# Optimization experiments

Measured on AMD Instinct MI355X. Metric: run time of the kernel, lower is better.

The kernel has to match this reference:

```python
import jax, jax.numpy as jnp
import numpy as np


def _masked(scores, mask):
    return jnp.where(mask == 0, -jnp.inf, scores)


def setup_inputs() -> dict:
    key = jax.random.key(0)
    ks = jax.random.split(key, 4)
    B, H, S, D = 2, 12, 4096, 64
    blk = 64
    nb = S // blk          # 64 blocks
    nw = nb - 2            # 62 windows
    R = 3                  # random blocks per window
    return {
        'query': jax.random.normal(ks[0], (B, H, S, D), dtype=jnp.float32),
        'key': jax.random.normal(ks[1], (B, H, S, D), dtype=jnp.float32),
        'value': jax.random.normal(ks[2], (B, H, S, D), dtype=jnp.float32),
        'q_mask': jnp.ones((B, 1, S, 1), dtype=jnp.float32),
        'kv_mask': jnp.ones((B, 1, 1, S), dtype=jnp.float32),
        'band_mask': jnp.ones((B, 1, nb - 4, blk, 3 * blk), dtype=jnp.float32),
        'q_block_mask': jnp.ones((B, nb, blk), dtype=jnp.float32),
        'kv_block_mask': jnp.ones((B, nb, blk), dtype=jnp.float32),
        'random_attn': jax.random.randint(ks[3], (H, nw, R), 0, nb, dtype=jnp.int32),
        'q_block_size': blk,
        'kv_block_size': blk,
    }


def reference(query, key, value, q_mask, kv_mask, band_mask, q_block_mask,
              kv_block_mask, random_attn, q_block_size, kv_block_size):
    B, H, S, D = query.shape
    Skv = key.shape[2]
    qb, kb = q_block_size, kv_block_size
    nb, nkb = S // qb, Skv // kb
    scale = 1.0 / (D ** 0.5)

    # expand random indices over batch: [B,H,nw,R]
    ra = jnp.broadcast_to(random_attn[None].astype(jnp.int32),
                          (B,) + random_attn.shape)
    nw, R = ra.shape[2], ra.shape[3]
    bidx = jnp.arange(B)[:, None, None, None]
    hidx = jnp.arange(H)[None, :, None, None]

    # random mask: [B,H,nw,qb,R*kb]
    rm = kv_block_mask[bidx, ra].reshape(B, H, nw, R * kb)
    random_mask = jnp.einsum('blq,bhlk->bhlqk', q_block_mask[:, 1:-1], rm)

    bq = query.reshape(B, H, nb, qb, D)
    bk = key.reshape(B, H, nkb, kb, D)
    bv = value.reshape(B, H, nkb, kb, D)

    # gathered random blocks: [B,H,nw,R*kb,D]
    sk = bk[bidx, hidx, ra].reshape(B, H, nw, R * kb, D)
    sv = bv[bidx, hidx, ra].reshape(B, H, nw, R * kb, D)

    # --- first query block: attends to everything ---
    p1 = jnp.einsum('bhqd,bhkd->bhqk', bq[:, :, 0], key) * scale
    a1 = jax.nn.softmax(_masked(p1, kv_mask), axis=-1)
    c1 = jnp.einsum('bhqk,bhkd->bhqd', a1, value)[:, :, None]

    # --- second query block ---
    k2 = jnp.concatenate([bk[:, :, 0], bk[:, :, 1], bk[:, :, 2], bk[:, :, -1],
                          sk[:, :, 0]], axis=2)
    v2 = jnp.concatenate([bv[:, :, 0], bv[:, :, 1], bv[:, :, 2], bv[:, :, -1],
                          sv[:, :, 0]], axis=2)
    p2 = jnp.einsum('bhqd,bhkd->bhqk', bq[:, :, 1], k2) * scale
    seq_pad = jnp.concatenate([kv_mask[:, :, :, :3 * kb],
                               kv_mask[:, :, :, -kb:],
                               jnp.ones_like(random_mask[:, :1, 0, :1])], axis=3)
    rand_pad = jnp.concatenate([jnp.ones_like(p2[:, :, :, :4 * kb]),
                                random_mask[:, :, 0]], axis=3)
    a2 = jax.nn.softmax(_masked(p2, jnp.minimum(seq_pad, rand_pad)), axis=-1)
    c2 = jnp.einsum('bhqk,bhkd->bhqd', a2, v2)[:, :, None]

    # --- middle blocks: window + global(first,last) + random ---
    ebk = jnp.concatenate([bk[:, :, 1:-3], bk[:, :, 2:-2], bk[:, :, 3:-1]], axis=3)
    ebv = jnp.concatenate([bv[:, :, 1:-3], bv[:, :, 2:-2], bv[:, :, 3:-1]], axis=3)
    mq = bq[:, :, 2:-2]  # [B,H,nb-4,qb,D]
    inner = _masked(jnp.einsum('bhlqd,bhlkd->bhlqk', mq, ebk) * scale, band_mask)
    randp = _masked(jnp.einsum('bhlqd,bhlkd->bhlqk', mq, sk[:, :, 1:-1]) * scale,
                    random_mask[:, :, 1:-1])
    fop = _masked(jnp.einsum('bhlqd,bhkd->bhlqk', mq, bk[:, :, 0]) * scale,
                  kv_mask[:, :, :, :kb][:, :, :, None, :])
    lop = _masked(jnp.einsum('bhlqd,bhkd->bhlqk', mq, bk[:, :, -1]) * scale,
                  kv_mask[:, :, :, -kb:][:, :, :, None, :])
    band = jnp.concatenate([fop, inner, lop, randp], axis=-1)
    aw = jax.nn.softmax(band, axis=-1)
    cm = jnp.einsum('bhlqk,bhlkd->bhlqd', aw[..., kb:4 * kb], ebv)
    cm += jnp.einsum('bhlqk,bhlkd->bhlqd', aw[..., 4 * kb:-kb], sv[:, :, 1:-1])
    cm += jnp.einsum('bhlqk,bhkd->bhlqd', aw[..., :kb], bv[:, :, 0])
    cm += jnp.einsum('bhlqk,bhkd->bhlqd', aw[..., -kb:], bv[:, :, -1])

    # --- second-to-last query block ---
    k3 = jnp.concatenate([bk[:, :, 0], bk[:, :, -3], bk[:, :, -2], bk[:, :, -1],
                          sk[:, :, -1]], axis=2)
    v3 = jnp.concatenate([bv[:, :, 0], bv[:, :, -3], bv[:, :, -2], bv[:, :, -1],
                          sv[:, :, -1]], axis=2)
    p3 = jnp.einsum('bhqd,bhkd->bhqk', bq[:, :, -2], k3) * scale
    seq_pad3 = jnp.concatenate([kv_mask[:, :, :, :kb],
                                kv_mask[:, :, :, -3 * kb:],
                                jnp.ones_like(random_mask[:, :1, 0, :1])], axis=3)
    rand_pad3 = jnp.concatenate([jnp.ones_like(p3[:, :, :, :4 * kb]),
                                 random_mask[:, :, -1]], axis=3)
    a3 = jax.nn.softmax(_masked(p3, jnp.minimum(seq_pad3, rand_pad3)), axis=-1)
    c3 = jnp.einsum('bhqk,bhkd->bhqd', a3, v3)[:, :, None]

    # --- last query block: attends to everything ---
    p4 = jnp.einsum('bhqd,bhkd->bhqk', bq[:, :, -1], key) * scale
    a4 = jax.nn.softmax(_masked(p4, kv_mask), axis=-1)
    c4 = jnp.einsum('bhqk,bhkd->bhqd', a4, value)[:, :, None]

    ctx = jnp.concatenate([c1, c2, cm, c3, c4], axis=2)
    return ctx.reshape(B, H, S, D) * q_mask
```

## Files before the change

kernel.cpp:

```cpp
#include <hip/hip_runtime.h>
#include <hip/hip_bf16.h>

#define BB 2
#define HH 12
#define SS 4096
#define DD 64
#define NB_ 64
#define NW_ 62
#define RR 3

#define PARTIAL_FLOATS 4160
#define N_HEAVY_UNITS  (BB * HH * 2)
#define N_CHUNKS       8
#define N_TILES        (BB * HH * NB_)
#define TILE_ELEMS     4096

using short8 = __attribute__((ext_vector_type(8))) short;
using f32x4  = __attribute__((ext_vector_type(4))) float;

__device__ __forceinline__ int swz(int r, int c) {
    return (r << 6) + ((((c >> 3) ^ r) & 7) << 3) + (c & 7);
}

__device__ __forceinline__ short pack_bf16(float f) {
    __bf16 b = (__bf16)f;
    return (short)__builtin_bit_cast(unsigned short, b);
}

__device__ __forceinline__ short8 load_cvt8_scaled(const float* p, float sc) {
    f32x4 a = *(const f32x4*)p;
    f32x4 b = *(const f32x4*)(p + 4);
    short8 r;
#pragma unroll
    for (int i = 0; i < 4; ++i) {
        r[i]     = pack_bf16(a[i] * sc);
        r[i + 4] = pack_bf16(b[i] * sc);
    }
    return r;
}

__global__ __launch_bounds__(256)
void bigbird_prepass(const float* __restrict__ K, const float* __restrict__ V,
                     short* __restrict__ Kfrag, short* __restrict__ Vfrag)
{
    const int tile = blockIdx.x;
    const int tid  = threadIdx.x;
    const size_t gbase = (size_t)tile * TILE_ELEMS;

#pragma unroll
    for (int rep = 0; rep < 2; ++rep) {
        const int p  = tid + rep * 256;
        const int f  = p >> 6;
        const int l  = p & 63;
        {
            const int key = (f >> 1) * 16 + (l & 15);
            const int d0  = ((l >> 4) << 3) + (f & 1) * 32;
            const float* kp = K + gbase + key * 64 + d0;
            f32x4 a = *(const f32x4*)(kp);
            f32x4 b = *(const f32x4*)(kp + 4);
            short8 s;
#pragma unroll
            for (int i = 0; i < 4; ++i) { s[i] = pack_bf16(a[i]); s[i + 4] = pack_bf16(b[i]); }
            *(short8*)&Kfrag[gbase + p * 8] = s;
        }
        {
            const int drow = (f >> 1) * 16 + (l & 15);
            const int key0 = ((l >> 4) << 3) + (f & 1) * 32;
            const float* vp = V + gbase + key0 * 64 + drow;
            short8 s;
#pragma unroll
            for (int e = 0; e < 8; ++e) s[e] = pack_bf16(vp[e * 64]);
            *(short8*)&Vfrag[gbase + p * 8] = s;
        }
    }
}

__global__ __launch_bounds__(256, 2)
void bigbird_main_frag(const short* __restrict__ Kfrag, const short* __restrict__ Vfrag,
                       const float* __restrict__ Q, const float* __restrict__ qmask,
                       const int* __restrict__ ra, float* __restrict__ Out,
                       float* __restrict__ part)
{
    __shared__ __align__(16) short PB[4][16 * 64];

    const int tid  = threadIdx.x;
    const int w    = tid >> 6;
    const int lane = tid & 63;
    const int g    = lane >> 4;
    const int m    = lane & 15;

    const int idx    = blockIdx.x;
    const int NHEAVY = N_HEAVY_UNITS * N_CHUNKS;

    bool heavy;
    int  b, h, qb, u = 0, chunk_base = 0, chunk = 0, nlist;
    int  r0 = 0, r1 = 0, r2 = 0;

    if (idx < NHEAVY) {
        heavy = true;
        const int slot = idx & 7;
        const int rest = idx >> 3;
        const int bh   = slot + 8 * (rest % 3);
        const int rem  = rest / 3;
        const int hb   = rem >> 3;
        chunk = rem & 7; chunk_base = chunk * 8; nlist = 8;
        u  = bh * 2 + hb;
        b  = bh / HH; h = bh % HH;
        qb = hb ? (NB_ - 1) : 0;
    } else {
        heavy = false;
        const int l   = idx - NHEAVY;
        const int bh  = (l & 7) + 8 * ((l >> 3) % 3);
        const int qidx = l / 24;
        b = bh / HH; h = bh % HH;
        qb = qidx + 1;
        const int* rp = ra + (h * NW_ + (qb - 1)) * RR;
        r0 = rp[0]; r1 = rp[1]; r2 = rp[2];
        nlist = (qb == 1 || qb == NB_ - 2) ? 7 : 8;
    }

    auto kb_s = [&](int ti) -> int {
        if (heavy) return chunk_base + ti;
        if (qb == 1)
            return ti == 0 ? 0 : ti == 1 ? 1 : ti == 2 ? 2 : ti == 3 ? 63
                 : ti == 4 ? r0 : ti == 5 ? r1 : r2;
        if (qb == NB_ - 2)
            return ti == 0 ? 0 : ti == 1 ? 61 : ti == 2 ? 62 : ti == 3 ? 63
                 : ti == 4 ? r0 : ti == 5 ? r1 : r2;
        return ti == 0 ? 0 : ti == 1 ? qb - 1 : ti == 2 ? qb : ti == 3 ? qb + 1
             : ti == 4 ? 63 : ti == 5 ? r0 : ti == 6 ? r1 : r2;
    };
    auto kb_v = [&](int ti) -> int {
        if (heavy) return chunk_base + ti;
        if (qb == 1 || qb == NB_ - 2) return kb_s(ti);
        return ti == 0 ? 0 : ti == 1 ? qb - 1 : ti == 2 ? qb : ti == 3 ? qb + 1
             : ti == 4 ? r0 : ti == 5 ? r1 : ti == 6 ? r2 : 63;
    };

    const int    bh_lin = b * HH + h;
    const size_t base   = (size_t)bh_lin * SS * DD;
    const short* Kbh    = Kfrag + (size_t)bh_lin * NB_ * TILE_ELEMS + (lane << 3);
    const short* Vbh    = Vfrag + (size_t)bh_lin * NB_ * TILE_ELEMS + (lane << 3);

    short8 qa[2];
    {
        const float* qp = Q + base + (size_t)(qb * 64 + w * 16 + m) * DD + g * 8;
        qa[0] = load_cvt8_scaled(qp, 0.125f);
        qa[1] = load_cvt8_scaled(qp + 32, 0.125f);
    }

    f32x4 oacc[4];
#pragma unroll
    for (int t = 0; t < 4; ++t) oacc[t] = (f32x4){0.f, 0.f, 0.f, 0.f};
    float lsum[4] = {0.f, 0.f, 0.f, 0.f};

    auto iter = [&](short8 (&kc)[8], short8 (&kn)[8], int t) {
        short8 vf[8];
        {
            const short* vp = Vbh + (size_t)kb_v(t) * TILE_ELEMS;
#pragma unroll
            for (int f = 0; f < 8; ++f) vf[f] = *(const short8*)(vp + f * 512);
        }

        f32x4 sacc[4];
#pragma unroll
        for (int q = 0; q < 4; ++q) sacc[q] = (f32x4){0.f, 0.f, 0.f, 0.f};
        __builtin_amdgcn_s_setprio(1);
#pragma unroll
        for (int ks = 0; ks < 2; ++ks)
#pragma unroll
            for (int q = 0; q < 4; ++q)
                sacc[q] = __builtin_amdgcn_mfma_f32_16x16x32_bf16(qa[ks], kc[q * 2 + ks], sacc[q], 0, 0, 0);
        __builtin_amdgcn_s_setprio(0);

        if (t + 1 < nlist) {
            const short* np = Kbh + (size_t)kb_s(t + 1) * TILE_ELEMS;
#pragma unroll
            for (int f = 0; f < 8; ++f) kn[f] = *(const short8*)(np + f * 512);
        }

#pragma unroll
        for (int q = 0; q < 4; ++q)
#pragma unroll
            for (int j = 0; j < 4; ++j) {
                const float p = __expf(sacc[q][j]);
                lsum[j] += p;
                PB[w][swz(4 * g + j, q * 16 + m)] = pack_bf16(p);
            }

        __builtin_amdgcn_s_setprio(1);
#pragma unroll
        for (int ks = 0; ks < 2; ++ks) {
            short8 pa = *(short8*)&PB[w][swz(m, g * 8 + ks * 32)];
#pragma unroll
            for (int q = 0; q < 4; ++q)
                oacc[q] = __builtin_amdgcn_mfma_f32_16x16x32_bf16(pa, vf[q * 2 + ks], oacc[q], 0, 0, 0);
        }
        __builtin_amdgcn_s_setprio(0);
    };

    short8 kfA[8], kfB[8];
    {
        const short* kp0 = Kbh + (size_t)kb_s(0) * TILE_ELEMS;
#pragma unroll
        for (int f = 0; f < 8; ++f) kfA[f] = *(const short8*)(kp0 + f * 512);
    }

    for (int t = 0; t < nlist; t += 2) {
        iter(kfA, kfB, t);
        if (t + 1 < nlist) iter(kfB, kfA, t + 1);
    }

#pragma unroll
    for (int j = 0; j < 4; ++j)
#pragma unroll
        for (int off = 1; off < 16; off <<= 1) lsum[j] += __shfl_xor(lsum[j], off);

    if (heavy) {
        float* pb = part + (size_t)(u * N_CHUNKS + chunk) * PARTIAL_FLOATS;
#pragma unroll
        for (int j = 0; j < 4; ++j) {
            const int row = w * 16 + 4 * g + j;
#pragma unroll
            for (int q = 0; q < 4; ++q) pb[row * 64 + q * 16 + m] = oacc[q][j];
            if (m == 0) pb[4096 + row] = lsum[j];
        }
    } else {
#pragma unroll
        for (int j = 0; j < 4; ++j) {
            const int row = qb * 64 + w * 16 + 4 * g + j;
            const float sc = qmask[b * SS + row] / lsum[j];
            float* op = Out + base + (size_t)row * DD + m;
#pragma unroll
            for (int q = 0; q < 4; ++q) op[q * 16] = oacc[q][j] * sc;
        }
    }
}

template<bool SPLIT>
__global__ __launch_bounds__(256)
void bigbird_main_reg(const float* __restrict__ Q, const float* __restrict__ K,
                      const float* __restrict__ V, const float* __restrict__ qmask,
                      const int* __restrict__ ra, float* __restrict__ Out,
                      float* __restrict__ ws)
{
    __shared__ __align__(16) short KB[2][64 * 64];
    __shared__ __align__(16) short VT[2][64 * 64];
    __shared__ __align__(16) short PB[4][16 * 64];

    const int tid  = threadIdx.x;
    const int w    = tid >> 6;
    const int lane = tid & 63;
    const int g    = lane >> 4;
    const int m    = lane & 15;

    const int idx    = blockIdx.x;
    const int NHEAVY = SPLIT ? (N_HEAVY_UNITS * N_CHUNKS) : N_HEAVY_UNITS;

    bool heavy;
    int  b, h, qb, u = 0, chunk = 0, chunk_base = 0, nlist;
    int  slist[8], vlist[8];

    if (idx < NHEAVY) {
        heavy = true;
        if (SPLIT) { u = idx >> 3; chunk = idx & 7; chunk_base = chunk * 8; nlist = 8; }
        else       { u = idx; chunk_base = 0; nlist = NB_; }
        const int bh = u >> 1;
        b = bh / HH; h = bh % HH;
        qb = (u & 1) ? (NB_ - 1) : 0;
    } else {
        heavy = false;
        const int idx2 = idx - NHEAVY;
        const int qidx = idx2 / (BB * HH);
        const int bh   = idx2 % (BB * HH);
        b = bh / HH; h = bh % HH;
        qb = qidx + 1;
        const int* rp = ra + (h * NW_ + (qb - 1)) * RR;
        if (qb == 1) {
            slist[0] = 0; slist[1] = 1; slist[2] = 2; slist[3] = 63;
            slist[4] = rp[0]; slist[5] = rp[1]; slist[6] = rp[2]; nlist = 7;
#pragma unroll
            for (int i = 0; i < 7; ++i) vlist[i] = slist[i];
        } else if (qb == NB_ - 2) {
            slist[0] = 0; slist[1] = 61; slist[2] = 62; slist[3] = 63;
            slist[4] = rp[0]; slist[5] = rp[1]; slist[6] = rp[2]; nlist = 7;
#pragma unroll
            for (int i = 0; i < 7; ++i) vlist[i] = slist[i];
        } else {
            slist[0] = 0; slist[1] = qb - 1; slist[2] = qb; slist[3] = qb + 1;
            slist[4] = 63; slist[5] = rp[0]; slist[6] = rp[1]; slist[7] = rp[2];
            vlist[0] = 0; vlist[1] = qb - 1; vlist[2] = qb; vlist[3] = qb + 1;
            vlist[4] = rp[0]; vlist[5] = rp[1]; vlist[6] = rp[2]; vlist[7] = 63;
            nlist = 8;
        }
    }

    const size_t base = ((size_t)(b * HH + h)) * SS * DD;

    short8 qa[2];
    {
        const float* qp = Q + base + (size_t)(qb * 64 + w * 16 + m) * DD + g * 8;
        qa[0] = load_cvt8_scaled(qp, 0.125f);
        qa[1] = load_cvt8_scaled(qp + 32, 0.125f);
    }

    f32x4 oacc[4];
#pragma unroll
    for (int t = 0; t < 4; ++t) oacc[t] = (f32x4){0.f, 0.f, 0.f, 0.f};
    float lsum[4] = {0.f, 0.f, 0.f, 0.f};

    const int kr = tid >> 2;
    const int kc = (tid & 3) * 16;
    const int vp = tid & 31;
    const int vd = (tid >> 5) * 8;

    f32x4 kreg[4], vreg[4];
    auto load_kv = [&](int i) {
        const int kbs = heavy ? (chunk_base + i) : slist[i];
        const int kbv = heavy ? (chunk_base + i) : vlist[i];
        const float* kp = K + base + (size_t)(kbs * 64 + kr) * DD + kc;
        kreg[0] = *(const f32x4*)(kp);
        kreg[1] = *(const f32x4*)(kp + 4);
        kreg[2] = *(const f32x4*)(kp + 8);
        kreg[3] = *(const f32x4*)(kp + 12);
        const float* vp0 = V + base + (size_t)(kbv * 64 + 2 * vp) * DD + vd;
        vreg[0] = *(const f32x4*)(vp0);
        vreg[1] = *(const f32x4*)(vp0 + 4);
        vreg[2] = *(const f32x4*)(vp0 + DD);
        vreg[3] = *(const f32x4*)(vp0 + DD + 4);
    };

    load_kv(0);
    int cur = 0;

    for (int it = 0; it < nlist; ++it) {
        {
            short8 s0, s1;
#pragma unroll
            for (int i = 0; i < 4; ++i) {
                s0[i] = pack_bf16(kreg[0][i]); s0[i + 4] = pack_bf16(kreg[1][i]);
                s1[i] = pack_bf16(kreg[2][i]); s1[i + 4] = pack_bf16(kreg[3][i]);
            }
            *(short8*)&KB[cur][swz(kr, kc)]     = s0;
            *(short8*)&KB[cur][swz(kr, kc + 8)] = s1;
#pragma unroll
            for (int i = 0; i < 8; ++i) {
                float f0 = (i < 4) ? vreg[0][i] : vreg[1][i - 4];
                float f1 = (i < 4) ? vreg[2][i] : vreg[3][i - 4];
                unsigned int pk = (unsigned int)(unsigned short)pack_bf16(f0) |
                                  ((unsigned int)(unsigned short)pack_bf16(f1) << 16);
                *(unsigned int*)&VT[cur][swz(vd + i, 2 * vp)] = pk;
            }
        }

        __syncthreads();

        if (it + 1 < nlist) load_kv(it + 1);

        f32x4 sacc[4];
#pragma unroll
        for (int t = 0; t < 4; ++t) sacc[t] = (f32x4){0.f, 0.f, 0.f, 0.f};
        __builtin_amdgcn_s_setprio(1);
#pragma unroll
        for (int ks = 0; ks < 2; ++ks) {
#pragma unroll
            for (int t = 0; t < 4; ++t) {
                short8 bk = *(short8*)&KB[cur][swz(t * 16 + m, g * 8 + ks * 32)];
                sacc[t] = __builtin_amdgcn_mfma_f32_16x16x32_bf16(qa[ks], bk, sacc[t], 0, 0, 0);
            }
        }
        __builtin_amdgcn_s_setprio(0);

#pragma unroll
        for (int t = 0; t < 4; ++t) {
#pragma unroll
            for (int j = 0; j < 4; ++j) {
                const float p = __expf(sacc[t][j]);
                lsum[j] += p;
                PB[w][swz(4 * g + j, t * 16 + m)] = pack_bf16(p);
            }
        }

        __builtin_amdgcn_s_setprio(1);
#pragma unroll
        for (int ks = 0; ks < 2; ++ks) {
            short8 pa = *(short8*)&PB[w][swz(m, g * 8 + ks * 32)];
#pragma unroll
            for (int t = 0; t < 4; ++t) {
                short8 bv = *(short8*)&VT[cur][swz(t * 16 + m, g * 8 + ks * 32)];
                oacc[t] = __builtin_amdgcn_mfma_f32_16x16x32_bf16(pa, bv, oacc[t], 0, 0, 0);
            }
        }
        __builtin_amdgcn_s_setprio(0);

        cur ^= 1;
    }

#pragma unroll
    for (int j = 0; j < 4; ++j)
#pragma unroll
        for (int off = 1; off < 16; off <<= 1) lsum[j] += __shfl_xor(lsum[j], off);

    if (SPLIT && heavy) {
        float* pb = ws + (size_t)(u * N_CHUNKS + chunk) * PARTIAL_FLOATS;
#pragma unroll
        for (int j = 0; j < 4; ++j) {
            const int row = w * 16 + 4 * g + j;
#pragma unroll
            for (int t = 0; t < 4; ++t) pb[row * 64 + t * 16 + m] = oacc[t][j];
            if (m == 0) pb[4096 + row] = lsum[j];
        }
    } else {
#pragma unroll
        for (int j = 0; j < 4; ++j) {
            const int row = qb * 64 + w * 16 + 4 * g + j;
            const float sc = qmask[b * SS + row] / lsum[j];
            float* op = Out + base + (size_t)row * DD + m;
#pragma unroll
            for (int t = 0; t < 4; ++t) op[t * 16] = oacc[t][j] * sc;
        }
    }
}

__global__ __launch_bounds__(256)
void bigbird_combine(const float* __restrict__ ws, const float* __restrict__ qmask,
                     float* __restrict__ Out)
{
    const int u  = blockIdx.x;
    const int bh = u >> 1;
    const int b  = bh / HH;
    const int h  = bh % HH;
    const int qb = (u & 1) ? (NB_ - 1) : 0;

    const int tid = threadIdx.x;
    const int r   = tid >> 2;
    const int s   = tid & 3;

    const float* pb0 = ws + (size_t)u * N_CHUNKS * PARTIAL_FLOATS;

    float L = 0.f;
    f32x4 o0 = {0,0,0,0}, o1 = {0,0,0,0}, o2 = {0,0,0,0}, o3 = {0,0,0,0};
#pragma unroll
    for (int c = 0; c < N_CHUNKS; ++c) {
        const float* pb = pb0 + c * PARTIAL_FLOATS;
        L += pb[4096 + r];
        const float* orow = pb + r * 64 + s * 16;
        f32x4 a0 = *(const f32x4*)(orow);
        f32x4 a1 = *(const f32x4*)(orow + 4);
        f32x4 a2 = *(const f32x4*)(orow + 8);
        f32x4 a3 = *(const f32x4*)(orow + 12);
#pragma unroll
        for (int i = 0; i < 4; ++i) {
            o0[i] += a0[i]; o1[i] += a1[i];
            o2[i] += a2[i]; o3[i] += a3[i];
        }
    }

    const int row = qb * 64 + r;
    const float scme = qmask[b * SS + row] / L;
    float* op = Out + ((size_t)(b * HH + h)) * SS * DD + (size_t)row * DD + s * 16;
#pragma unroll
    for (int i = 0; i < 4; ++i) { o0[i] *= scme; o1[i] *= scme; o2[i] *= scme; o3[i] *= scme; }
    *(f32x4*)(op)      = o0;
    *(f32x4*)(op + 4)  = o1;
    *(f32x4*)(op + 8)  = o2;
    *(f32x4*)(op + 12) = o3;
}

extern "C" void kernel_launch(void* const* d_in, const int* in_sizes, int n_in,
                              void* d_out, int out_size, void* d_ws, size_t ws_size,
                              hipStream_t stream) {
    const float* Q     = (const float*)d_in[0];
    const float* K     = (const float*)d_in[1];
    const float* V     = (const float*)d_in[2];
    const float* qmask = (const float*)d_in[3];
    const int*   ra    = (const int*)d_in[8];
    float* Out = (float*)d_out;

    const size_t img_bytes  = (size_t)N_TILES * TILE_ELEMS * sizeof(short);
    const size_t part_bytes = (size_t)N_HEAVY_UNITS * N_CHUNKS * PARTIAL_FLOATS * sizeof(float);
    const size_t need_img   = 2 * img_bytes + part_bytes;

    if (ws_size >= need_img) {
        short* Kfrag = (short*)d_ws;
        short* Vfrag = Kfrag + (size_t)N_TILES * TILE_ELEMS;
        float* part  = (float*)((char*)d_ws + 2 * img_bytes);
        bigbird_prepass<<<N_TILES, 256, 0, stream>>>(K, V, Kfrag, Vfrag);
        const int grid = N_HEAVY_UNITS * N_CHUNKS + BB * HH * (NB_ - 2);
        bigbird_main_frag<<<grid, 256, 0, stream>>>(Kfrag, Vfrag, Q, qmask, ra, Out, part);
        bigbird_combine<<<N_HEAVY_UNITS, 256, 0, stream>>>((const float*)part, qmask, Out);
    } else if (ws_size >= part_bytes) {
        float* ws = (float*)d_ws;
        const int grid = N_HEAVY_UNITS * N_CHUNKS + BB * HH * (NB_ - 2);
        bigbird_main_reg<true><<<grid, 256, 0, stream>>>(Q, K, V, qmask, ra, Out, ws);
        bigbird_combine<<<N_HEAVY_UNITS, 256, 0, stream>>>((const float*)ws, qmask, Out);
    } else {
        float* ws = (float*)d_ws;
        const int grid = N_HEAVY_UNITS + BB * HH * (NB_ - 2);
        bigbird_main_reg<false><<<grid, 256, 0, stream>>>(Q, K, V, qmask, ra, Out, ws);
    }
}
```

Measured before the change: 62.96 us.

## Split key dimension across warps in main kernel and reduce partial outputs in LDS

The main attention kernel now has each of the four warps handle 16 keys of each 64-key tile for all 64 query rows, instead of each warp handling 16 query rows over all keys. The V image is re-laid out to match, and each warp loads only its slice of K/V per tile, which cuts per-warp register and load traffic. In exchange it adds a cross-warp reduction of the output accumulators and row sums through shared memory, with several __syncthreads, and a larger accumulator footprint (16 f32x4 per lane). It also folds log2(e) into the Q scale so exp2 replaces expf, and drops setprio in the fallback kernel.

```diff
diff --git a/kernel.cpp b/kernel.cpp
--- a/kernel.cpp
+++ b/kernel.cpp
@@ -41,7 +41,7 @@
 
 __global__ __launch_bounds__(256)
 void bigbird_prepass(const float* __restrict__ K, const float* __restrict__ V,
-                     short* __restrict__ Kfrag, short* __restrict__ Vfrag)
+                     short* __restrict__ Kimg, short* __restrict__ Vimg)
 {
     const int tile = blockIdx.x;
     const int tid  = threadIdx.x;
@@ -49,39 +49,41 @@
 
 #pragma unroll
     for (int rep = 0; rep < 2; ++rep) {
-        const int p  = tid + rep * 256;
-        const int f  = p >> 6;
-        const int l  = p & 63;
+        const int p = tid + rep * 256;
         {
-            const int key = (f >> 1) * 16 + (l & 15);
-            const int d0  = ((l >> 4) << 3) + (f & 1) * 32;
-            const float* kp = K + gbase + key * 64 + d0;
+            const int f = p >> 6, l = p & 63;
+            const int sl = f >> 1, ks = f & 1;
+            const float* kp = K + gbase + (size_t)(16 * sl + (l & 15)) * 64
+                            + (l >> 4) * 8 + 32 * ks;
             f32x4 a = *(const f32x4*)(kp);
             f32x4 b = *(const f32x4*)(kp + 4);
             short8 s;
 #pragma unroll
             for (int i = 0; i < 4; ++i) { s[i] = pack_bf16(a[i]); s[i + 4] = pack_bf16(b[i]); }
-            *(short8*)&Kfrag[gbase + p * 8] = s;
+            *(short8*)&Kimg[gbase + (size_t)p * 8] = s;
         }
         {
-            const int drow = (f >> 1) * 16 + (l & 15);
-            const int key0 = ((l >> 4) << 3) + (f & 1) * 32;
-            const float* vp = V + gbase + key0 * 64 + drow;
+            const int f = p >> 5, l = p & 31;
+            const int sl = f >> 2, dt = f & 3;
+            const int d  = 16 * dt + (l & 15);
+            const int k0 = 16 * sl + (l >> 4) * 8;
+            const float* vp = V + gbase + (size_t)k0 * 64 + d;
             short8 s;
 #pragma unroll
             for (int e = 0; e < 8; ++e) s[e] = pack_bf16(vp[e * 64]);
-            *(short8*)&Vfrag[gbase + p * 8] = s;
+            *(short8*)&Vimg[gbase + (size_t)p * 8] = s;
         }
     }
 }
 
 __global__ __launch_bounds__(256, 2)
-void bigbird_main_frag(const short* __restrict__ Kfrag, const short* __restrict__ Vfrag,
-                       const float* __restrict__ Q, const float* __restrict__ qmask,
-                       const int* __restrict__ ra, float* __restrict__ Out,
-                       float* __restrict__ part)
+void bigbird_main_ks(const short* __restrict__ Kimg, const short* __restrict__ Vimg,
+                     const float* __restrict__ Q, const float* __restrict__ qmask,
+                     const int* __restrict__ ra, float* __restrict__ Out,
+                     float* __restrict__ part)
 {
-    __shared__ __align__(16) short PB[4][16 * 64];
+    __shared__ __align__(16) short PBn[4][64 * 32];
+    __shared__ float LB[4 * 64];
 
     const int tid  = threadIdx.x;
     const int w    = tid >> 6;
@@ -139,82 +141,143 @@
 
     const int    bh_lin = b * HH + h;
     const size_t base   = (size_t)bh_lin * SS * DD;
-    const short* Kbh    = Kfrag + (size_t)bh_lin * NB_ * TILE_ELEMS + (lane << 3);
-    const short* Vbh    = Vfrag + (size_t)bh_lin * NB_ * TILE_ELEMS + (lane << 3);
-
-    short8 qa[2];
+    const short* Kbh    = Kimg + (size_t)bh_lin * NB_ * TILE_ELEMS;
+    const short* Vbh    = Vimg + (size_t)bh_lin * NB_ * TILE_ELEMS;
+
+    const short8 vzero = {0, 0, 0, 0, 0, 0, 0, 0};
+
     {
-        const float* qp = Q + base + (size_t)(qb * 64 + w * 16 + m) * DD + g * 8;
-        qa[0] = load_cvt8_scaled(qp, 0.125f);
-        qa[1] = load_cvt8_scaled(qp + 32, 0.125f);
-    }
-
-    f32x4 oacc[4];
-#pragma unroll
-    for (int t = 0; t < 4; ++t) oacc[t] = (f32x4){0.f, 0.f, 0.f, 0.f};
-    float lsum[4] = {0.f, 0.f, 0.f, 0.f};
-
-    auto iter = [&](short8 (&kc)[8], short8 (&kn)[8], int t) {
-        short8 vf[8];
-        {
-            const short* vp = Vbh + (size_t)kb_v(t) * TILE_ELEMS;
-#pragma unroll
-            for (int f = 0; f < 8; ++f) vf[f] = *(const short8*)(vp + f * 512);
-        }
-
+        const int row = lane;
+        const int s2  = (row >> 2) & 3;
+        *(short8*)&PBn[w][row * 32 + ((2 ^ s2) << 3)] = vzero;
+        *(short8*)&PBn[w][row * 32 + ((3 ^ s2) << 3)] = vzero;
+    }
+
+    short8 qa[4][2];
+    {
+        const float qsc = 0.125f * 1.44269504088896f;
+#pragma unroll
+        for (int qt = 0; qt < 4; ++qt) {
+            const float* qp = Q + base + (size_t)(qb * 64 + qt * 16 + m) * DD + g * 8;
+            qa[qt][0] = load_cvt8_scaled(qp, qsc);
+            qa[qt][1] = load_cvt8_scaled(qp + 32, qsc);
+        }
+    }
+
+    f32x4 oacc[4][4];
+#pragma unroll
+    for (int qt = 0; qt < 4; ++qt)
+#pragma unroll
+        for (int dt = 0; dt < 4; ++dt) oacc[qt][dt] = (f32x4){0.f, 0.f, 0.f, 0.f};
+    float lsum16[16];
+#pragma unroll
+    for (int i = 0; i < 16; ++i) lsum16[i] = 0.f;
+
+    auto loadK = [&](short8 (&kf)[2], int t) {
+        const short* p = Kbh + (size_t)kb_s(t) * TILE_ELEMS + ((w * 2) << 9) + (lane << 3);
+        kf[0] = *(const short8*)(p);
+        kf[1] = *(const short8*)(p + 512);
+    };
+    auto loadV = [&](short8 (&vf)[4], int t) {
+        const short* p = Vbh + (size_t)kb_v(t) * TILE_ELEMS + ((w * 4) << 8) + (lane << 3);
+#pragma unroll
+        for (int dt = 0; dt < 4; ++dt)
+            vf[dt] = (lane < 32) ? *(const short8*)(p + dt * 256) : vzero;
+    };
+
+    auto iter = [&](short8 (&kc)[2], short8 (&vc)[4],
+                    short8 (&kn)[2], short8 (&vn)[4], int t) {
         f32x4 sacc[4];
 #pragma unroll
-        for (int q = 0; q < 4; ++q) sacc[q] = (f32x4){0.f, 0.f, 0.f, 0.f};
+        for (int qt = 0; qt < 4; ++qt) sacc[qt] = (f32x4){0.f, 0.f, 0.f, 0.f};
         __builtin_amdgcn_s_setprio(1);
 #pragma unroll
         for (int ks = 0; ks < 2; ++ks)
 #pragma unroll
-            for (int q = 0; q < 4; ++q)
-                sacc[q] = __builtin_amdgcn_mfma_f32_16x16x32_bf16(qa[ks], kc[q * 2 + ks], sacc[q], 0, 0, 0);
+            for (int qt = 0; qt < 4; ++qt)
+                sacc[qt] = __builtin_amdgcn_mfma_f32_16x16x32_bf16(qa[qt][ks], kc[ks], sacc[qt], 0, 0, 0);
         __builtin_amdgcn_s_setprio(0);
 
-        if (t + 1 < nlist) {
-            const short* np = Kbh + (size_t)kb_s(t + 1) * TILE_ELEMS;
-#pragma unroll
-            for (int f = 0; f < 8; ++f) kn[f] = *(const short8*)(np + f * 512);
-        }
-
-#pragma unroll
-        for (int q = 0; q < 4; ++q)
+        if (t + 1 < nlist) { loadK(kn, t + 1); loadV(vn, t + 1); }
+
+#pragma unroll
+        for (int qt = 0; qt < 4; ++qt)
 #pragma unroll
             for (int j = 0; j < 4; ++j) {
-                const float p = __expf(sacc[q][j]);
-                lsum[j] += p;
-                PB[w][swz(4 * g + j, q * 16 + m)] = pack_bf16(p);
+                const float p = __builtin_amdgcn_exp2f(sacc[qt][j]);
+                lsum16[qt * 4 + j] += p;
+                const int row = 16 * qt + 4 * g + j;
+                const int c   = (m >> 3) ^ ((row >> 2) & 3);
+                PBn[w][row * 32 + (c << 3) + (m & 7)] = pack_bf16(p);
             }
 
         __builtin_amdgcn_s_setprio(1);
 #pragma unroll
-        for (int ks = 0; ks < 2; ++ks) {
-            short8 pa = *(short8*)&PB[w][swz(m, g * 8 + ks * 32)];
-#pragma unroll
-            for (int q = 0; q < 4; ++q)
-                oacc[q] = __builtin_amdgcn_mfma_f32_16x16x32_bf16(pa, vf[q * 2 + ks], oacc[q], 0, 0, 0);
+        for (int qt = 0; qt < 4; ++qt) {
+            const int row = 16 * qt + m;
+            const int cc  = g ^ ((row >> 2) & 3);
+            short8 pa = *(short8*)&PBn[w][row * 32 + (cc << 3)];
+#pragma unroll
+            for (int dt = 0; dt < 4; ++dt)
+                oacc[qt][dt] = __builtin_amdgcn_mfma_f32_16x16x32_bf16(pa, vc[dt], oacc[qt][dt], 0, 0, 0);
         }
         __builtin_amdgcn_s_setprio(0);
     };
 
-    short8 kfA[8], kfB[8];
-    {
-        const short* kp0 = Kbh + (size_t)kb_s(0) * TILE_ELEMS;
-#pragma unroll
-        for (int f = 0; f < 8; ++f) kfA[f] = *(const short8*)(kp0 + f * 512);
-    }
-
+    short8 kA[2], kB[2], vA[4], vB[4];
+    loadK(kA, 0); loadV(vA, 0);
     for (int t = 0; t < nlist; t += 2) {
-        iter(kfA, kfB, t);
-        if (t + 1 < nlist) iter(kfB, kfA, t + 1);
-    }
-
-#pragma unroll
-    for (int j = 0; j < 4; ++j)
-#pragma unroll
-        for (int off = 1; off < 16; off <<= 1) lsum[j] += __shfl_xor(lsum[j], off);
+        iter(kA, vA, kB, vB, t);
+        if (t + 1 < nlist) iter(kB, vB, kA, vA, t + 1);
+    }
+
+#pragma unroll
+    for (int i = 0; i < 16; ++i) {
+        lsum16[i] += __shfl_xor(lsum16[i], 1);
+        lsum16[i] += __shfl_xor(lsum16[i], 2);
+        lsum16[i] += __shfl_xor(lsum16[i], 4);
+        lsum16[i] += __shfl_xor(lsum16[i], 8);
+    }
+    if (m == 0) {
+#pragma unroll
+        for (int qt = 0; qt < 4; ++qt)
+#pragma unroll
+            for (int j = 0; j < 4; ++j)
+                LB[w * 64 + qt * 16 + g * 4 + j] = lsum16[qt * 4 + j];
+    }
+    __syncthreads();
+
+    float* OB = (float*)&PBn[0][0];
+    float fin[16];
+#pragma unroll
+    for (int i = 0; i < 16; ++i) fin[i] = 0.f;
+
+#pragma unroll
+    for (int ph = 0; ph < 4; ++ph) {
+#pragma unroll
+        for (int dt = 0; dt < 4; ++dt)
+#pragma unroll
+            for (int j = 0; j < 4; ++j)
+                OB[(w * 64 + lane) * 16 + dt * 4 + j] = oacc[ph][dt][j];
+        __syncthreads();
+        if (w == ph) {
+#pragma unroll
+            for (int w2 = 0; w2 < 4; ++w2)
+#pragma unroll
+                for (int dt = 0; dt < 4; ++dt)
+#pragma unroll
+                    for (int j = 0; j < 4; ++j)
+                        fin[dt * 4 + j] += OB[(w2 * 64 + lane) * 16 + dt * 4 + j];
+        }
+        __syncthreads();
+    }
+
+    float Lt[4];
+#pragma unroll
+    for (int j = 0; j < 4; ++j) {
+        const int row = w * 16 + 4 * g + j;
+        Lt[j] = LB[row] + LB[64 + row] + LB[128 + row] + LB[192 + row];
+    }
 
     if (heavy) {
         float* pb = part + (size_t)(u * N_CHUNKS + chunk) * PARTIAL_FLOATS;
@@ -222,17 +285,17 @@
         for (int j = 0; j < 4; ++j) {
             const int row = w * 16 + 4 * g + j;
 #pragma unroll
-            for (int q = 0; q < 4; ++q) pb[row * 64 + q * 16 + m] = oacc[q][j];
-            if (m == 0) pb[4096 + row] = lsum[j];
+            for (int dt = 0; dt < 4; ++dt) pb[row * 64 + dt * 16 + m] = fin[dt * 4 + j];
+            if (m == 0) pb[4096 + row] = Lt[j];
         }
     } else {
 #pragma unroll
         for (int j = 0; j < 4; ++j) {
             const int row = qb * 64 + w * 16 + 4 * g + j;
-            const float sc = qmask[b * SS + row] / lsum[j];
+            const float sc = qmask[b * SS + row] / Lt[j];
             float* op = Out + base + (size_t)row * DD + m;
 #pragma unroll
-            for (int q = 0; q < 4; ++q) op[q * 16] = oacc[q][j] * sc;
+            for (int dt = 0; dt < 4; ++dt) op[dt * 16] = fin[dt * 4 + j] * sc;
         }
     }
 }
@@ -300,8 +363,9 @@
     short8 qa[2];
     {
         const float* qp = Q + base + (size_t)(qb * 64 + w * 16 + m) * DD + g * 8;
-        qa[0] = load_cvt8_scaled(qp, 0.125f);
-        qa[1] = load_cvt8_scaled(qp + 32, 0.125f);
+        const float qsc = 0.125f * 1.44269504088896f;
+        qa[0] = load_cvt8_scaled(qp, qsc);
+        qa[1] = load_cvt8_scaled(qp + 32, qsc);
     }
 
     f32x4 oacc[4];
@@ -360,7 +424,6 @@
         f32x4 sacc[4];
 #pragma unroll
         for (int t = 0; t < 4; ++t) sacc[t] = (f32x4){0.f, 0.f, 0.f, 0.f};
-        __builtin_amdgcn_s_setprio(1);
 #pragma unroll
         for (int ks = 0; ks < 2; ++ks) {
 #pragma unroll
@@ -369,19 +432,17 @@
                 sacc[t] = __builtin_amdgcn_mfma_f32_16x16x32_bf16(qa[ks], bk, sacc[t], 0, 0, 0);
             }
         }
-        __builtin_amdgcn_s_setprio(0);
 
 #pragma unroll
         for (int t = 0; t < 4; ++t) {
 #pragma unroll
             for (int j = 0; j < 4; ++j) {
-                const float p = __expf(sacc[t][j]);
+                const float p = __builtin_amdgcn_exp2f(sacc[t][j]);
                 lsum[j] += p;
                 PB[w][swz(4 * g + j, t * 16 + m)] = pack_bf16(p);
             }
         }
 
-        __builtin_amdgcn_s_setprio(1);
 #pragma unroll
         for (int ks = 0; ks < 2; ++ks) {
             short8 pa = *(short8*)&PB[w][swz(m, g * 8 + ks * 32)];
@@ -391,7 +452,6 @@
                 oacc[t] = __builtin_amdgcn_mfma_f32_16x16x32_bf16(pa, bv, oacc[t], 0, 0, 0);
             }
         }
-        __builtin_amdgcn_s_setprio(0);
 
         cur ^= 1;
     }
@@ -482,12 +542,12 @@
     const size_t need_img   = 2 * img_bytes + part_bytes;
 
     if (ws_size >= need_img) {
-        short* Kfrag = (short*)d_ws;
-        short* Vfrag = Kfrag + (size_t)N_TILES * TILE_ELEMS;
-        float* part  = (float*)((char*)d_ws + 2 * img_bytes);
-        bigbird_prepass<<<N_TILES, 256, 0, stream>>>(K, V, Kfrag, Vfrag);
+        short* Kimg = (short*)d_ws;
+        short* Vimg = Kimg + (size_t)N_TILES * TILE_ELEMS;
+        float* part = (float*)((char*)d_ws + 2 * img_bytes);
+        bigbird_prepass<<<N_TILES, 256, 0, stream>>>(K, V, Kimg, Vimg);
         const int grid = N_HEAVY_UNITS * N_CHUNKS + BB * HH * (NB_ - 2);
-        bigbird_main_frag<<<grid, 256, 0, stream>>>(Kfrag, Vfrag, Q, qmask, ra, Out, part);
+        bigbird_main_ks<<<grid, 256, 0, stream>>>(Kimg, Vimg, Q, qmask, ra, Out, part);
         bigbird_combine<<<N_HEAVY_UNITS, 256, 0, stream>>>((const float*)part, qmask, Out);
     } else if (ws_size >= part_bytes) {
         float* ws = (float*)d_ws;
```

Measured after the change: 80.74 us. 1.28x slower.
